# Performance work log

Hardware: AMD Instinct MI355X
Metric: run time of the kernel (lower is better)

## Reference

```python
import jax, jax.numpy as jnp
import numpy as np

IGNORE_INDEX = 255
NUM_CLASSES = 6


def setup_inputs() -> dict:
    key = jax.random.key(0)
    k1, k2 = jax.random.split(key)
    B, C, H, W = 16, 256, 128, 128
    x = jax.random.normal(k1, (B, C, H, W), dtype=jnp.float32)
    gt = jax.random.randint(k2, (B, 1, H, W), 0, NUM_CLASSES, dtype=jnp.int32)
    return {"x": x, "gt": gt}


def reference(x, gt):
    # x: (B, C, H, W) float32; gt: (B, 1, H, W) int
    B, C, H, W = x.shape
    K = NUM_CLASSES
    # F.interpolate(gt.float(), size=(H,W), mode='nearest') is identity here
    label = gt[:, 0]                                  # (B, H, W)
    not_ignore = (label != IGNORE_INDEX)              # (B, H, W) bool
    label = jnp.where(not_ignore, label, 0)           # zero out ignored pixels
    # one-hot with ignored positions masked to all-zero rows
    oh = jax.nn.one_hot(label, K, dtype=jnp.float32)  # (B, H, W, K)
    oh = oh * not_ignore[..., None].astype(jnp.float32)
    oh_flat = oh.reshape(B, H * W, K)                 # (B, N, K)
    x_flat = x.reshape(B, C, H * W)                   # (B, C, N)
    # per-class pixel counts (count_nonzero of one-hot == its sum)
    counts = jnp.sum(oh_flat, axis=1)                 # (B, K)
    counts = jnp.maximum(counts, 1.0)
    # masked sum pooling per class: (B, K, N) @ (B, N, C) -> (B, K, C)
    center = jnp.einsum('bnk,bcn->bkc', oh_flat, x_flat)
    center = center / counts[:, :, None]
    return center
```

## Files before the change

kernel.cpp:

```cpp
#include <hip/hip_runtime.h>
#include <hip/hip_bf16.h>

#define BATCH 16
#define CHAN  256
#define HW    16384
#define NCLS  6

typedef float  f32x4 __attribute__((ext_vector_type(4)));
typedef int    i32x4 __attribute__((ext_vector_type(4)));

__global__ __launch_bounds__(256)
void gt2center_kernel(const float* __restrict__ x,
                      const int*   __restrict__ gt,
                      float*       __restrict__ out) {
    const int bc = blockIdx.x;
    const int b  = bc >> 8;
    const int c  = bc & 255;
    const float* __restrict__ xp = x  + (size_t)bc * HW;
    const int*   __restrict__ gp = gt + (size_t)b  * HW;
    const int t = threadIdx.x;

    float s[NCLS];
    int   cnt[NCLS];
#pragma unroll
    for (int k = 0; k < NCLS; ++k) { s[k] = 0.0f; cnt[k] = 0; }

#pragma unroll 4
    for (int i = 0; i < 16; ++i) {
        const int n = i * 1024 + t * 4;
        const f32x4 v = *reinterpret_cast<const f32x4*>(xp + n);
        const i32x4 L = *reinterpret_cast<const i32x4*>(gp + n);
#pragma unroll
        for (int k = 0; k < NCLS; ++k) {
            s[k] += (L.x == k) ? v.x : 0.0f;
            s[k] += (L.y == k) ? v.y : 0.0f;
            s[k] += (L.z == k) ? v.z : 0.0f;
            s[k] += (L.w == k) ? v.w : 0.0f;
            cnt[k] += (L.x == k) + (L.y == k) + (L.z == k) + (L.w == k);
        }
    }

#pragma unroll
    for (int off = 32; off >= 1; off >>= 1) {
#pragma unroll
        for (int k = 0; k < NCLS; ++k) {
            s[k]   += __shfl_xor(s[k],   off, 64);
            cnt[k] += __shfl_xor(cnt[k], off, 64);
        }
    }

    __shared__ float ls[4][NCLS];
    __shared__ int   lc[4][NCLS];
    const int wave = t >> 6, lane = t & 63;
    if (lane == 0) {
#pragma unroll
        for (int k = 0; k < NCLS; ++k) { ls[wave][k] = s[k]; lc[wave][k] = cnt[k]; }
    }
    __syncthreads();

    if (t < NCLS) {
        const float ssum = ls[0][t] + ls[1][t] + ls[2][t] + ls[3][t];
        const int   csum = lc[0][t] + lc[1][t] + lc[2][t] + lc[3][t];
        const float d = (csum > 1) ? (float)csum : 1.0f;
        out[((size_t)b * NCLS + t) * CHAN + c] = ssum / d;
    }
}

extern "C" void kernel_launch(void* const* d_in, const int* in_sizes, int n_in,
                              void* d_out, int out_size, void* d_ws, size_t ws_size,
                              hipStream_t stream) {
    const float* x   = (const float*)d_in[0];
    const int*   gt  = (const int*)d_in[1];
    float*       out = (float*)d_out;
    gt2center_kernel<<<BATCH * CHAN, 256, 0, stream>>>(x, gt, out);
}
```

Measured before the change: 53.15 us.

## Pack labels to bytes in a pre-pass to cut label read traffic

Adds a small pre-kernel that packs the int32 label map into uint8 in the workspace. The main reduction kernel then reads 4 labels per 32-bit load instead of 16 bytes. This cuts the per-block label traffic, which every channel block re-reads from cache, by a factor of four. It also fully unrolls the main loop and adds an occupancy hint to launch bounds. The cost is an extra kernel launch and a workspace write/read pass over the labels.

```diff
diff --git a/kernel.cpp b/kernel.cpp
--- a/kernel.cpp
+++ b/kernel.cpp
@@ -10,14 +10,25 @@
 typedef int    i32x4 __attribute__((ext_vector_type(4)));
 
 __global__ __launch_bounds__(256)
+void compress_kernel(const int* __restrict__ gt, unsigned char* __restrict__ g8) {
+    const int idx = (blockIdx.x * 256 + threadIdx.x) * 4;
+    const i32x4 L = *reinterpret_cast<const i32x4*>(gt + idx);
+    unsigned int packed = (unsigned int)(L.x & 0xff)
+                        | ((unsigned int)(L.y & 0xff) << 8)
+                        | ((unsigned int)(L.z & 0xff) << 16)
+                        | ((unsigned int)(L.w & 0xff) << 24);
+    *reinterpret_cast<unsigned int*>(g8 + idx) = packed;
+}
+
+__global__ __launch_bounds__(256, 4)
 void gt2center_kernel(const float* __restrict__ x,
-                      const int*   __restrict__ gt,
-                      float*       __restrict__ out) {
+                      const unsigned char* __restrict__ g8,
+                      float* __restrict__ out) {
     const int bc = blockIdx.x;
     const int b  = bc >> 8;
     const int c  = bc & 255;
     const float* __restrict__ xp = x  + (size_t)bc * HW;
-    const int*   __restrict__ gp = gt + (size_t)b  * HW;
+    const unsigned char* __restrict__ gp = g8 + (size_t)b * HW;
     const int t = threadIdx.x;
 
     float s[NCLS];
@@ -25,18 +36,22 @@
 #pragma unroll
     for (int k = 0; k < NCLS; ++k) { s[k] = 0.0f; cnt[k] = 0; }
 
-#pragma unroll 4
+#pragma unroll
     for (int i = 0; i < 16; ++i) {
         const int n = i * 1024 + t * 4;
         const f32x4 v = *reinterpret_cast<const f32x4*>(xp + n);
-        const i32x4 L = *reinterpret_cast<const i32x4*>(gp + n);
+        const unsigned int Lw = *reinterpret_cast<const unsigned int*>(gp + n);
+        const int l0 = Lw & 0xff;
+        const int l1 = (Lw >> 8) & 0xff;
+        const int l2 = (Lw >> 16) & 0xff;
+        const int l3 = Lw >> 24;
 #pragma unroll
         for (int k = 0; k < NCLS; ++k) {
-            s[k] += (L.x == k) ? v.x : 0.0f;
-            s[k] += (L.y == k) ? v.y : 0.0f;
-            s[k] += (L.z == k) ? v.z : 0.0f;
-            s[k] += (L.w == k) ? v.w : 0.0f;
-            cnt[k] += (L.x == k) + (L.y == k) + (L.z == k) + (L.w == k);
+            s[k] += (l0 == k) ? v.x : 0.0f;
+            s[k] += (l1 == k) ? v.y : 0.0f;
+            s[k] += (l2 == k) ? v.z : 0.0f;
+            s[k] += (l3 == k) ? v.w : 0.0f;
+            cnt[k] += (l0 == k) + (l1 == k) + (l2 == k) + (l3 == k);
         }
     }
 
@@ -72,5 +87,8 @@
     const float* x   = (const float*)d_in[0];
     const int*   gt  = (const int*)d_in[1];
     float*       out = (float*)d_out;
-    gt2center_kernel<<<BATCH * CHAN, 256, 0, stream>>>(x, gt, out);
+    unsigned char* g8 = (unsigned char*)d_ws;
+
+    compress_kernel<<<(BATCH * HW) / 1024, 256, 0, stream>>>(gt, g8);
+    gt2center_kernel<<<BATCH * CHAN, 256, 0, stream>>>(x, g8, out);
 }
```

New measurement: 59.26 us. 11.5% more time.
